# Kernel tuning notes

Measured on AMD Instinct MI355X. Metric: run time of the kernel, lower is better.

## Reference

```python
import jax, jax.numpy as jnp
import numpy as np

B, L, S, H, E, D = 2, 2048, 2048, 16, 64, 64


def setup_inputs() -> dict:
    key = jax.random.key(0)
    kq, kk, kv = jax.random.split(key, 3)
    queries = jax.random.normal(kq, (B, L, H, E), dtype=jnp.float32)
    keys = jax.random.normal(kk, (B, S, H, E), dtype=jnp.float32)
    values = jax.random.normal(kv, (B, S, H, D), dtype=jnp.float32)
    # causal mask: True = masked out (matches masked_fill semantics)
    causal = jnp.triu(jnp.ones((L, S), dtype=bool), k=1)
    attn_mask = jnp.broadcast_to(causal, (B, L, S))
    return {"queries": queries, "keys": keys, "values": values, "attn_mask": attn_mask}


def reference(queries, keys, values, attn_mask):
    # queries: [B,L,H,E], keys: [B,S,H,E], values: [B,S,H,D], attn_mask: [B,L,S] bool
    E_ = queries.shape[-1]
    scale = 1.0 / jnp.sqrt(jnp.asarray(E_, dtype=queries.dtype))
    scores = jnp.einsum('blhe,bshe->bhls', queries, keys)  # [B,H,L,S]
    scores = jnp.where(attn_mask[:, None, :, :], -jnp.inf, scores)
    A = jax.nn.softmax(scale * scores, axis=-1)
    A = jnp.nan_to_num(A)  # fully-masked rows -> 0 (dropout prob is 0.0)
    V = jnp.einsum('bhls,bshd->blhd', A, values)  # [B,L,H,D]
    return (V, A)
```

## Files before the change

kernel.cpp:

```cpp
#include <hip/hip_runtime.h>
#include <cstdint>
#include <cstddef>

#define B_ 2
#define L_ 2048
#define S_ 2048
#define H_ 16
#define E_ 64
#define D_ 64

#define LOG2E_SCALE 0.18033688011112042f

typedef __attribute__((ext_vector_type(8))) short short8;
typedef __attribute__((ext_vector_type(4))) float float4v;
typedef __attribute__((ext_vector_type(4))) unsigned short ushort4v;
typedef __attribute__((ext_vector_type(2))) unsigned int uint2v;

__device__ __forceinline__ unsigned short f2bf(float f) {
  unsigned u = __builtin_bit_cast(unsigned, f);
  u += 0x7FFFu + ((u >> 16) & 1u);
  return (unsigned short)(u >> 16);
}

__device__ __forceinline__ float myexp2(float x) {
#if __has_builtin(__builtin_amdgcn_exp2f)
  return __builtin_amdgcn_exp2f(x);
#else
  return exp2f(x);
#endif
}

__global__ __launch_bounds__(256)
void conv_qk_kernel(const float* __restrict__ Qi, const float* __restrict__ Ki,
                    unsigned short* __restrict__ Qo, unsigned short* __restrict__ Ko) {
  const unsigned bx = blockIdx.x;
  const float* in = (bx & 1u) ? Ki : Qi;
  unsigned short* out = (bx & 1u) ? Ko : Qo;
  unsigned idx4 = (bx >> 1) * 256u + threadIdx.x;
  unsigned e4 = idx4 & 15u;
  unsigned h  = (idx4 >> 4) & 15u;
  unsigned n  = (idx4 >> 8) & 2047u;
  unsigned b  = idx4 >> 19;
  float4v v = *(const float4v*)(in + (size_t)idx4 * 4u);
  ushort4v o;
  o.x = f2bf(v.x); o.y = f2bf(v.y); o.z = f2bf(v.z); o.w = f2bf(v.w);
  *(ushort4v*)(out + (((size_t)(b * H_ + h) * 2048u + n) * 16u + e4) * 4u) = o;
}

__global__ __launch_bounds__(256)
void conv_vt_kernel(const float* __restrict__ V, unsigned short* __restrict__ VT) {
  __shared__ float tile[64 * 65];
  const int st = blockIdx.x, h = blockIdx.y, b = blockIdx.z;
  const int tid = threadIdx.x;
  const float* vb = V + ((size_t)(b * S_ + st * 64) * H_ + h) * D_;
  #pragma unroll
  for (int i = 0; i < 4; ++i) {
    int e = tid + i * 256;
    int row = e >> 4, c4 = (e & 15) * 4;
    float4v v = *(const float4v*)(vb + (size_t)row * (H_ * D_) + c4);
    tile[row * 65 + c4 + 0] = v.x; tile[row * 65 + c4 + 1] = v.y;
    tile[row * 65 + c4 + 2] = v.z; tile[row * 65 + c4 + 3] = v.w;
  }
  __syncthreads();
  #pragma unroll
  for (int i = 0; i < 4; ++i) {
    int e = tid + i * 256;
    int d = e >> 4, c4 = (e & 15) * 4;
    ushort4v o;
    o.x = f2bf(tile[(c4 + 0) * 65 + d]); o.y = f2bf(tile[(c4 + 1) * 65 + d]);
    o.z = f2bf(tile[(c4 + 2) * 65 + d]); o.w = f2bf(tile[(c4 + 3) * 65 + d]);
    *(ushort4v*)(VT + ((size_t)(b * H_ + h) * D_ + d) * S_ + st * 64 + c4) = o;
  }
}

__global__ __launch_bounds__(256, 4)
void fullattn10_kernel(const unsigned short* __restrict__ Qbf,
                       const unsigned short* __restrict__ Kbf,
                       const unsigned short* __restrict__ VT,
                       float* __restrict__ OutV, float* __restrict__ OutA) {
  __shared__ alignas(16) char smem[18944];
  unsigned short* Ps = (unsigned short*)smem;
  float* Lbuf = (float*)(smem + 18432);
  float* Obuf = (float*)smem;

  const int tid = threadIdx.x;
  const int w = tid >> 6;
  const int lane = tid & 63;
  const int quad = lane >> 4;
  const int n16 = lane & 15;

  const unsigned bid = blockIdx.x;
  const unsigned xcd = bid & 7u;
  const unsigned slot = bid >> 3;
  const unsigned g = xcd * 4u + (slot >> 6);
  const unsigned p = slot & 63u;
  const int h = (int)(g & 15u), b = (int)(g >> 4);
  const int stA = (int)p;
  const int stB = 127 - stA;
  const int jtA = stA >> 2, doffA = (stA & 3) * 16;
  const int jtB = stB >> 2, doffB = (stB & 3) * 16;

  const unsigned short* kbase = Kbf + (size_t)(b * H_ + h) * S_ * E_;
  const unsigned short* vbase = VT + (size_t)(b * H_ + h) * D_ * S_;

  float* arowA = OutA + ((size_t)((b * H_ + h) * L_) + stA * 16) * (size_t)S_;
  float* arowB = OutA + ((size_t)((b * H_ + h) * L_) + stB * 16) * (size_t)S_;

  auto zfill = [&](float* arow0, int jt) {
    const int c4start = (jt + 1) * 16;
    #pragma unroll
    for (int i = 0; i < 4; ++i) {
      float4v* rp = (float4v*)(arow0 + (size_t)(w * 4 + i) * S_);
      for (int c4 = c4start + lane; c4 < S_ / 4; c4 += 64) {
        float4v z = {0.f, 0.f, 0.f, 0.f};
        __builtin_nontemporal_store(z, rp + c4);
      }
    }
  };
  zfill(arowA, jtA);
  zfill(arowB, jtB);

  const unsigned short* qrowA = Qbf + ((size_t)(b * H_ + h) * L_ + stA * 16 + n16) * E_;
  const short8 qA0 = *(const short8*)(qrowA + quad * 8);
  const short8 qA1 = *(const short8*)(qrowA + 32 + quad * 8);
  const unsigned short* qrowB = Qbf + ((size_t)(b * H_ + h) * L_ + stB * 16 + n16) * E_;
  const short8 qB0 = *(const short8*)(qrowB + quad * 8);
  const short8 qB1 = *(const short8*)(qrowB + 32 + quad * 8);

  auto pass1 = [&](int jt, int doff, short8 q0, short8 q1) -> float {
    float ls = 0.f;
    short8 kA0[4], kA1[4], kB0[4], kB1[4];
    auto loadK = [&](int j, short8 (&c0)[4], short8 (&c1)[4]) {
      const unsigned short* kb = kbase + (size_t)j * 64 * E_;
      #pragma unroll
      for (int t = 0; t < 4; ++t) {
        const unsigned short* kr = kb + (size_t)(t * 16 + n16) * E_;
        c0[t] = *(const short8*)(kr + quad * 8);
        c1[t] = *(const short8*)(kr + 32 + quad * 8);
      }
    };
    auto procK = [&](const short8 (&c0)[4], const short8 (&c1)[4], int j) {
      #pragma unroll
      for (int t = 0; t < 4; ++t) {
        float4v acc = {0.f, 0.f, 0.f, 0.f};
        acc = __builtin_amdgcn_mfma_f32_16x16x32_bf16(c0[t], q0, acc, 0, 0, 0);
        acc = __builtin_amdgcn_mfma_f32_16x16x32_bf16(c1[t], q1, acc, 0, 0, 0);
        #pragma unroll
        for (int r = 0; r < 4; ++r) {
          float x = acc[r] * LOG2E_SCALE;
          if (j == jt && (t * 16 + quad * 4 + r > doff + n16)) x = -__builtin_inff();
          ls += myexp2(x);
        }
      }
    };
    if (w <= jt) {
      loadK(w, kA0, kA1);
      int j = w;
      for (;;) {
        if (j + 4 <= jt) loadK(j + 4, kB0, kB1);
        procK(kA0, kA1, j);
        j += 4;
        if (j > jt) break;
        if (j + 4 <= jt) loadK(j + 4, kA0, kA1);
        procK(kB0, kB1, j);
        j += 4;
        if (j > jt) break;
      }
    }
    return ls;
  };

  float lsA = pass1(jtA, doffA, qA0, qA1);
  float lsB = pass1(jtB, doffB, qB0, qB1);
  lsA += __shfl_xor(lsA, 16); lsA += __shfl_xor(lsA, 32);
  lsB += __shfl_xor(lsB, 16); lsB += __shfl_xor(lsB, 32);
  if (quad == 0) { Lbuf[w * 16 + n16] = lsA; Lbuf[64 + w * 16 + n16] = lsB; }
  __syncthreads();
  const float invA = 1.0f / (Lbuf[n16] + Lbuf[16 + n16] + Lbuf[32 + n16] + Lbuf[48 + n16]);
  const float invB = 1.0f / (Lbuf[64 + n16] + Lbuf[80 + n16] + Lbuf[96 + n16] + Lbuf[112 + n16]);

  auto pass2 = [&](int jt, int doff, short8 q0, short8 q1, float inv_l,
                   float* arow0, float4v (&oacc)[4]) {
    float* arowL = arow0 + (size_t)n16 * S_ + quad * 4;
    int par = 0;
    for (int j = w; j <= jt; j += 4, par ^= 1) {
      short8 v0f[4], v1f[4];
      #pragma unroll
      for (int t2 = 0; t2 < 4; ++t2) {
        const unsigned short* vr = vbase + (size_t)(t2 * 16 + n16) * S_ + j * 64;
        v0f[t2] = *(const short8*)(vr + quad * 8);
        v1f[t2] = *(const short8*)(vr + 32 + quad * 8);
      }
      const unsigned short* kb = kbase + (size_t)j * 64 * E_;
      unsigned short* psw = Ps + (size_t)((w << 1) | par) * (16 * 72);
      #pragma unroll
      for (int t = 0; t < 4; ++t) {
        const unsigned short* kr = kb + (size_t)(t * 16 + n16) * E_;
        const short8 c0 = *(const short8*)(kr + quad * 8);
        const short8 c1 = *(const short8*)(kr + 32 + quad * 8);
        float4v acc = {0.f, 0.f, 0.f, 0.f};
        acc = __builtin_amdgcn_mfma_f32_16x16x32_bf16(c0, q0, acc, 0, 0, 0);
        acc = __builtin_amdgcn_mfma_f32_16x16x32_bf16(c1, q1, acc, 0, 0, 0);
        float p4v[4];
        #pragma unroll
        for (int r = 0; r < 4; ++r) {
          p4v[r] = myexp2(acc[r] * LOG2E_SCALE) * inv_l;
          if (j == jt && (t * 16 + quad * 4 + r > doff + n16)) p4v[r] = 0.f;
        }
        float4v p4 = {p4v[0], p4v[1], p4v[2], p4v[3]};
        __builtin_nontemporal_store(p4, (float4v*)(arowL + j * 64 + t * 16));
        uint2v dw;
        dw.x = (unsigned)f2bf(p4v[0]) | ((unsigned)f2bf(p4v[1]) << 16);
        dw.y = (unsigned)f2bf(p4v[2]) | ((unsigned)f2bf(p4v[3]) << 16);
        *(uint2v*)&psw[n16 * 72 + t * 16 + quad * 4] = dw;
      }
      __builtin_amdgcn_wave_barrier();
      const short8 aP0 = *(const short8*)&psw[n16 * 72 + quad * 8];
      const short8 aP1 = *(const short8*)&psw[n16 * 72 + 32 + quad * 8];
      #pragma unroll
      for (int t2 = 0; t2 < 4; ++t2) {
        oacc[t2] = __builtin_amdgcn_mfma_f32_16x16x32_bf16(aP0, v0f[t2], oacc[t2], 0, 0, 0);
        oacc[t2] = __builtin_amdgcn_mfma_f32_16x16x32_bf16(aP1, v1f[t2], oacc[t2], 0, 0, 0);
      }
    }
  };

  auto combineO = [&](int l0, float4v (&oacc)[4]) {
    __syncthreads();
    #pragma unroll
    for (int t2 = 0; t2 < 4; ++t2)
      #pragma unroll
      for (int r = 0; r < 4; ++r)
        Obuf[(size_t)(w * 16 + quad * 4 + r) * 68 + t2 * 16 + n16] = oacc[t2][r];
    __syncthreads();
    const int row = tid >> 4;
    const int c0 = (tid & 15) * 4;
    float4v s = *(const float4v*)&Obuf[(size_t)row * 68 + c0];
    #pragma unroll
    for (int ww = 1; ww < 4; ++ww) {
      float4v t = *(const float4v*)&Obuf[(size_t)(ww * 16 + row) * 68 + c0];
      s.x += t.x; s.y += t.y; s.z += t.z; s.w += t.w;
    }
    float* op = OutV + ((size_t)(b * L_ + l0 + row) * H_ + h) * D_ + c0;
    __builtin_nontemporal_store(s, (float4v*)op);
    __syncthreads();
  };

  float4v oacc[4];
  #pragma unroll
  for (int t2 = 0; t2 < 4; ++t2) oacc[t2] = (float4v){0.f, 0.f, 0.f, 0.f};
  pass2(jtA, doffA, qA0, qA1, invA, arowA, oacc);
  combineO(stA * 16, oacc);

  #pragma unroll
  for (int t2 = 0; t2 < 4; ++t2) oacc[t2] = (float4v){0.f, 0.f, 0.f, 0.f};
  pass2(jtB, doffB, qB0, qB1, invB, arowB, oacc);
  combineO(stB * 16, oacc);
}

__global__ __launch_bounds__(256, 4)
void fullattn_fb_kernel(const float* __restrict__ Q, const float* __restrict__ K,
                        const float* __restrict__ V, float* __restrict__ OutV,
                        float* __restrict__ OutA) {
  __shared__ alignas(16) unsigned short Qs[64 * 72];
  __shared__ alignas(16) unsigned short Ks[64 * 72];
  __shared__ alignas(16) unsigned short VTs[64 * 72];
  __shared__ alignas(16) unsigned short Ps[64 * 72];
  const int tid = threadIdx.x;
  const int w = tid >> 6, lane = tid & 63, quad = lane >> 4, n16 = lane & 15;
  const int lt = (int)(gridDim.x - 1u - blockIdx.x);
  const int h = blockIdx.y, b = blockIdx.z;
  const int l0 = lt * 64;
  float* arow0 = OutA + ((size_t)((b * H_ + h) * L_) + l0) * (size_t)S_;
  {
    const int c4start = (lt + 1) * 16;
    for (int rr = w; rr < 64; rr += 4) {
      float4v* rp = (float4v*)(arow0 + (size_t)rr * S_);
      for (int c4 = c4start + lane; c4 < S_ / 4; c4 += 64) {
        float4v z = {0.f, 0.f, 0.f, 0.f};
        __builtin_nontemporal_store(z, rp + c4);
      }
    }
  }
  {
    const float* qb = Q + ((size_t)(b * L_ + l0) * H_ + h) * E_;
    #pragma unroll
    for (int i = 0; i < 4; ++i) {
      int e = tid + i * 256;
      int row = e >> 4, c4 = (e & 15) * 4;
      float4v qv = *(const float4v*)(qb + (size_t)row * (H_ * E_) + c4);
      ushort4v o; o.x = f2bf(qv.x); o.y = f2bf(qv.y); o.z = f2bf(qv.z); o.w = f2bf(qv.w);
      *(ushort4v*)&Qs[row * 72 + c4] = o;
    }
  }
  auto stageK = [&](int j) {
    const float* kb = K + ((size_t)(b * S_ + j * 64) * H_ + h) * E_;
    #pragma unroll
    for (int i = 0; i < 4; ++i) {
      int e = tid + i * 256;
      int row = e >> 4, c4 = (e & 15) * 4;
      float4v kv = *(const float4v*)(kb + (size_t)row * (H_ * E_) + c4);
      ushort4v o; o.x = f2bf(kv.x); o.y = f2bf(kv.y); o.z = f2bf(kv.z); o.w = f2bf(kv.w);
      *(ushort4v*)&Ks[row * 72 + c4] = o;
    }
  };
  auto stageV = [&](int j) {
    const float* vb = V + ((size_t)(b * S_ + j * 64) * H_ + h) * D_;
    const int d = lane;
    #pragma unroll
    for (int i = 0; i < 8; ++i) {
      int s2 = w * 8 + i;
      float f0 = vb[(size_t)(2 * s2) * (H_ * D_) + d];
      float f1 = vb[(size_t)(2 * s2 + 1) * (H_ * D_) + d];
      unsigned pk = (unsigned)f2bf(f0) | ((unsigned)f2bf(f1) << 16);
      *(unsigned*)&VTs[d * 72 + 2 * s2] = pk;
    }
  };
  __syncthreads();
  const short8 aQ0 = *(const short8*)&Qs[(w * 16 + n16) * 72 + quad * 8];
  const short8 aQ1 = *(const short8*)&Qs[(w * 16 + n16) * 72 + 32 + quad * 8];
  float m2[4], lsum[4];
  #pragma unroll
  for (int r = 0; r < 4; ++r) { m2[r] = -__builtin_inff(); lsum[r] = 0.f; }
  for (int j = 0; j <= lt; ++j) {
    stageK(j);
    __syncthreads();
    float x[4][4];
    #pragma unroll
    for (int t = 0; t < 4; ++t) {
      const short8 b0 = *(const short8*)&Ks[(t * 16 + n16) * 72 + quad * 8];
      const short8 b1 = *(const short8*)&Ks[(t * 16 + n16) * 72 + 32 + quad * 8];
      float4v acc = {0.f, 0.f, 0.f, 0.f};
      acc = __builtin_amdgcn_mfma_f32_16x16x32_bf16(aQ0, b0, acc, 0, 0, 0);
      acc = __builtin_amdgcn_mfma_f32_16x16x32_bf16(aQ1, b1, acc, 0, 0, 0);
      #pragma unroll
      for (int r = 0; r < 4; ++r) x[t][r] = acc[r] * LOG2E_SCALE;
    }
    if (j == lt) {
      #pragma unroll
      for (int t = 0; t < 4; ++t)
        #pragma unroll
        for (int r = 0; r < 4; ++r)
          if (t * 16 + n16 > w * 16 + quad * 4 + r) x[t][r] = -__builtin_inff();
    }
    #pragma unroll
    for (int r = 0; r < 4; ++r) {
      float mx = fmaxf(fmaxf(x[0][r], x[1][r]), fmaxf(x[2][r], x[3][r]));
      #pragma unroll
      for (int off = 8; off >= 1; off >>= 1) mx = fmaxf(mx, __shfl_xor(mx, off));
      float mnew = fmaxf(m2[r], mx);
      float alpha = myexp2(m2[r] - mnew);
      float sm = myexp2(x[0][r] - mnew) + myexp2(x[1][r] - mnew) +
                 myexp2(x[2][r] - mnew) + myexp2(x[3][r] - mnew);
      #pragma unroll
      for (int off = 8; off >= 1; off >>= 1) sm += __shfl_xor(sm, off);
      lsum[r] = lsum[r] * alpha + sm;
      m2[r] = mnew;
    }
    __syncthreads();
  }
  float inv_l[4];
  #pragma unroll
  for (int r = 0; r < 4; ++r) inv_l[r] = 1.0f / lsum[r];
  float4v oacc[4];
  #pragma unroll
  for (int t2 = 0; t2 < 4; ++t2) oacc[t2] = (float4v){0.f, 0.f, 0.f, 0.f};
  for (int j = 0; j <= lt; ++j) {
    stageK(j);
    stageV(j);
    __syncthreads();
    float* arow = arow0 + (size_t)(w * 16 + quad * 4) * S_ + j * 64 + n16;
    #pragma unroll
    for (int t = 0; t < 4; ++t) {
      const short8 b0 = *(const short8*)&Ks[(t * 16 + n16) * 72 + quad * 8];
      const short8 b1 = *(const short8*)&Ks[(t * 16 + n16) * 72 + 32 + quad * 8];
      float4v acc = {0.f, 0.f, 0.f, 0.f};
      acc = __builtin_amdgcn_mfma_f32_16x16x32_bf16(aQ0, b0, acc, 0, 0, 0);
      acc = __builtin_amdgcn_mfma_f32_16x16x32_bf16(aQ1, b1, acc, 0, 0, 0);
      #pragma unroll
      for (int r = 0; r < 4; ++r) {
        float p = myexp2(acc[r] * LOG2E_SCALE - m2[r]) * inv_l[r];
        if (j == lt && (t * 16 + n16 > w * 16 + quad * 4 + r)) p = 0.f;
        __builtin_nontemporal_store(p, arow + (size_t)r * S_ + t * 16);
        float pp = __shfl_xor(p, 1);
        unsigned short sp = f2bf(p), spp = f2bf(pp);
        unsigned dw = (n16 & 1) ? ((unsigned)spp | ((unsigned)sp << 16))
                                : ((unsigned)sp | ((unsigned)spp << 16));
        *(unsigned*)&Ps[(w * 16 + quad * 4 + r) * 72 + (t * 16 + (n16 & ~1))] = dw;
      }
    }
    __builtin_amdgcn_wave_barrier();
    const short8 aP0 = *(const short8*)&Ps[(w * 16 + n16) * 72 + quad * 8];
    const short8 aP1 = *(const short8*)&Ps[(w * 16 + n16) * 72 + 32 + quad * 8];
    #pragma unroll
    for (int t2 = 0; t2 < 4; ++t2) {
      const short8 v0 = *(const short8*)&VTs[(t2 * 16 + n16) * 72 + quad * 8];
      const short8 v1 = *(const short8*)&VTs[(t2 * 16 + n16) * 72 + 32 + quad * 8];
      oacc[t2] = __builtin_amdgcn_mfma_f32_16x16x32_bf16(aP0, v0, oacc[t2], 0, 0, 0);
      oacc[t2] = __builtin_amdgcn_mfma_f32_16x16x32_bf16(aP1, v1, oacc[t2], 0, 0, 0);
    }
    __syncthreads();
  }
  float* ob = OutV + ((size_t)(b * L_ + l0 + w * 16 + quad * 4) * H_ + h) * D_ + n16;
  #pragma unroll
  for (int t2 = 0; t2 < 4; ++t2)
    #pragma unroll
    for (int r = 0; r < 4; ++r)
      __builtin_nontemporal_store(oacc[t2][r], ob + (size_t)r * (H_ * D_) + t2 * 16);
}

extern "C" void kernel_launch(void* const* d_in, const int* in_sizes, int n_in,
                              void* d_out, int out_size, void* d_ws, size_t ws_size,
                              hipStream_t stream) {
  (void)in_sizes; (void)n_in; (void)out_size;
  const float* Q = (const float*)d_in[0];
  const float* K = (const float*)d_in[1];
  const float* V = (const float*)d_in[2];
  float* OutV = (float*)d_out;
  float* OutA = (float*)d_out + (size_t)B_ * L_ * H_ * D_;

  const size_t bytes_each = (size_t)B_ * H_ * 2048 * 64 * sizeof(unsigned short);
  if (ws_size >= 3 * bytes_each) {
    unsigned short* Qbf = (unsigned short*)d_ws;
    unsigned short* Kbf = (unsigned short*)((char*)d_ws + bytes_each);
    unsigned short* VTb = (unsigned short*)((char*)d_ws + 2 * bytes_each);
    const int nblk = (B_ * 2048 * H_ * E_ / 4) / 256;
    conv_qk_kernel<<<2 * nblk, 256, 0, stream>>>(Q, K, Qbf, Kbf);
    conv_vt_kernel<<<dim3(S_ / 64, H_, B_), 256, 0, stream>>>(V, VTb);
    fullattn10_kernel<<<2048, 256, 0, stream>>>(Qbf, Kbf, VTb, OutV, OutA);
  } else {
    fullattn_fb_kernel<<<dim3(L_ / 64, H_, B_), 256, 0, stream>>>(Q, K, V, OutV, OutA);
  }
}
```

Baseline: 739.4 us.

## Split softmax-denominator pass into separate kernel with workspace row sums

The fused attention kernel is split in two. A lightweight lpass_kernel computes the softmax denominators, writes their reciprocals to a workspace buffer and does the zero-fill of the masked upper triangle. The main kernel then reads those reciprocals and does only the probability/PV pass. The aim is to raise occupancy and shrink register pressure per kernel, with launch bounds of 8 and 5 instead of 4. It also drops the manual K double-buffering and the XCD-aware block remapping in favour of a plain 3D grid. The cost is an extra launch, a small workspace round trip, and a larger workspace requirement that could route to the fallback path if the workspace is too small.

After: 733.3 us. Within noise of the previous version (-0.8%).

```diff
diff --git a/kernel.cpp b/kernel.cpp
--- a/kernel.cpp
+++ b/kernel.cpp
@@ -73,15 +73,11 @@
   }
 }
 
-__global__ __launch_bounds__(256, 4)
-void fullattn10_kernel(const unsigned short* __restrict__ Qbf,
-                       const unsigned short* __restrict__ Kbf,
-                       const unsigned short* __restrict__ VT,
-                       float* __restrict__ OutV, float* __restrict__ OutA) {
-  __shared__ alignas(16) char smem[18944];
-  unsigned short* Ps = (unsigned short*)smem;
-  float* Lbuf = (float*)(smem + 18432);
-  float* Obuf = (float*)smem;
+__global__ __launch_bounds__(256, 8)
+void lpass_kernel(const unsigned short* __restrict__ Qbf,
+                  const unsigned short* __restrict__ Kbf,
+                  float* __restrict__ Lws, float* __restrict__ OutA) {
+  __shared__ float Lbuf[128];
 
   const int tid = threadIdx.x;
   const int w = tid >> 6;
@@ -89,20 +85,13 @@
   const int quad = lane >> 4;
   const int n16 = lane & 15;
 
-  const unsigned bid = blockIdx.x;
-  const unsigned xcd = bid & 7u;
-  const unsigned slot = bid >> 3;
-  const unsigned g = xcd * 4u + (slot >> 6);
-  const unsigned p = slot & 63u;
-  const int h = (int)(g & 15u), b = (int)(g >> 4);
-  const int stA = (int)p;
+  const int h = blockIdx.y, b = blockIdx.z;
+  const int stA = (int)blockIdx.x;
   const int stB = 127 - stA;
   const int jtA = stA >> 2, doffA = (stA & 3) * 16;
   const int jtB = stB >> 2, doffB = (stB & 3) * 16;
 
   const unsigned short* kbase = Kbf + (size_t)(b * H_ + h) * S_ * E_;
-  const unsigned short* vbase = VT + (size_t)(b * H_ + h) * D_ * S_;
-
   float* arowA = OutA + ((size_t)((b * H_ + h) * L_) + stA * 16) * (size_t)S_;
   float* arowB = OutA + ((size_t)((b * H_ + h) * L_) + stB * 16) * (size_t)S_;
 
@@ -120,31 +109,20 @@
   zfill(arowA, jtA);
   zfill(arowB, jtB);
 
-  const unsigned short* qrowA = Qbf + ((size_t)(b * H_ + h) * L_ + stA * 16 + n16) * E_;
-  const short8 qA0 = *(const short8*)(qrowA + quad * 8);
-  const short8 qA1 = *(const short8*)(qrowA + 32 + quad * 8);
-  const unsigned short* qrowB = Qbf + ((size_t)(b * H_ + h) * L_ + stB * 16 + n16) * E_;
-  const short8 qB0 = *(const short8*)(qrowB + quad * 8);
-  const short8 qB1 = *(const short8*)(qrowB + 32 + quad * 8);
-
-  auto pass1 = [&](int jt, int doff, short8 q0, short8 q1) -> float {
+  auto pass1 = [&](int jt, int doff, const unsigned short* qrow) -> float {
+    const short8 q0 = *(const short8*)(qrow + quad * 8);
+    const short8 q1 = *(const short8*)(qrow + 32 + quad * 8);
     float ls = 0.f;
-    short8 kA0[4], kA1[4], kB0[4], kB1[4];
-    auto loadK = [&](int j, short8 (&c0)[4], short8 (&c1)[4]) {
+    for (int j = w; j <= jt; j += 4) {
       const unsigned short* kb = kbase + (size_t)j * 64 * E_;
       #pragma unroll
       for (int t = 0; t < 4; ++t) {
         const unsigned short* kr = kb + (size_t)(t * 16 + n16) * E_;
-        c0[t] = *(const short8*)(kr + quad * 8);
-        c1[t] = *(const short8*)(kr + 32 + quad * 8);
-      }
-    };
-    auto procK = [&](const short8 (&c0)[4], const short8 (&c1)[4], int j) {
-      #pragma unroll
-      for (int t = 0; t < 4; ++t) {
+        const short8 c0 = *(const short8*)(kr + quad * 8);
+        const short8 c1 = *(const short8*)(kr + 32 + quad * 8);
         float4v acc = {0.f, 0.f, 0.f, 0.f};
-        acc = __builtin_amdgcn_mfma_f32_16x16x32_bf16(c0[t], q0, acc, 0, 0, 0);
-        acc = __builtin_amdgcn_mfma_f32_16x16x32_bf16(c1[t], q1, acc, 0, 0, 0);
+        acc = __builtin_amdgcn_mfma_f32_16x16x32_bf16(c0, q0, acc, 0, 0, 0);
+        acc = __builtin_amdgcn_mfma_f32_16x16x32_bf16(c1, q1, acc, 0, 0, 0);
         #pragma unroll
         for (int r = 0; r < 4; ++r) {
           float x = acc[r] * LOG2E_SCALE;
@@ -152,35 +130,61 @@
           ls += myexp2(x);
         }
       }
-    };
-    if (w <= jt) {
-      loadK(w, kA0, kA1);
-      int j = w;
-      for (;;) {
-        if (j + 4 <= jt) loadK(j + 4, kB0, kB1);
-        procK(kA0, kA1, j);
-        j += 4;
-        if (j > jt) break;
-        if (j + 4 <= jt) loadK(j + 4, kA0, kA1);
-        procK(kB0, kB1, j);
-        j += 4;
-        if (j > jt) break;
-      }
     }
     return ls;
   };
 
-  float lsA = pass1(jtA, doffA, qA0, qA1);
-  float lsB = pass1(jtB, doffB, qB0, qB1);
+  const unsigned short* qbase = Qbf + (size_t)(b * H_ + h) * L_ * E_;
+  float lsA = pass1(jtA, doffA, qbase + (size_t)(stA * 16 + n16) * E_);
+  float lsB = pass1(jtB, doffB, qbase + (size_t)(stB * 16 + n16) * E_);
   lsA += __shfl_xor(lsA, 16); lsA += __shfl_xor(lsA, 32);
   lsB += __shfl_xor(lsB, 16); lsB += __shfl_xor(lsB, 32);
   if (quad == 0) { Lbuf[w * 16 + n16] = lsA; Lbuf[64 + w * 16 + n16] = lsB; }
   __syncthreads();
-  const float invA = 1.0f / (Lbuf[n16] + Lbuf[16 + n16] + Lbuf[32 + n16] + Lbuf[48 + n16]);
-  const float invB = 1.0f / (Lbuf[64 + n16] + Lbuf[80 + n16] + Lbuf[96 + n16] + Lbuf[112 + n16]);
-
-  auto pass2 = [&](int jt, int doff, short8 q0, short8 q1, float inv_l,
-                   float* arow0, float4v (&oacc)[4]) {
+  if (tid < 32) {
+    const int row = tid & 15, s = tid >> 4;
+    const float* lb = Lbuf + s * 64;
+    const float sum = lb[row] + lb[16 + row] + lb[32 + row] + lb[48 + row];
+    const int st = s ? stB : stA;
+    Lws[(size_t)(b * H_ + h) * L_ + st * 16 + row] = 1.0f / sum;
+  }
+}
+
+__global__ __launch_bounds__(256, 5)
+void fullattn11_kernel(const unsigned short* __restrict__ Qbf,
+                       const unsigned short* __restrict__ Kbf,
+                       const unsigned short* __restrict__ VT,
+                       const float* __restrict__ Lws,
+                       float* __restrict__ OutV, float* __restrict__ OutA) {
+  __shared__ alignas(16) char smem[18432];
+  unsigned short* Ps = (unsigned short*)smem;
+  float* Obuf = (float*)smem;
+
+  const int tid = threadIdx.x;
+  const int w = tid >> 6;
+  const int lane = tid & 63;
+  const int quad = lane >> 4;
+  const int n16 = lane & 15;
+
+  const int h = blockIdx.y, b = blockIdx.z;
+  const int stA = (int)blockIdx.x;
+  const int stB = 127 - stA;
+  const int jtA = stA >> 2, doffA = (stA & 3) * 16;
+  const int jtB = stB >> 2, doffB = (stB & 3) * 16;
+
+  const unsigned short* kbase = Kbf + (size_t)(b * H_ + h) * S_ * E_;
+  const unsigned short* vbase = VT + (size_t)(b * H_ + h) * D_ * S_;
+  const unsigned short* qbase = Qbf + (size_t)(b * H_ + h) * L_ * E_;
+  const float* lrow = Lws + (size_t)(b * H_ + h) * L_;
+
+  float* arowA = OutA + ((size_t)((b * H_ + h) * L_) + stA * 16) * (size_t)S_;
+  float* arowB = OutA + ((size_t)((b * H_ + h) * L_) + stB * 16) * (size_t)S_;
+
+  auto pass2 = [&](int jt, int doff, int st, float* arow0, float4v (&oacc)[4]) {
+    const unsigned short* qrow = qbase + (size_t)(st * 16 + n16) * E_;
+    const short8 q0 = *(const short8*)(qrow + quad * 8);
+    const short8 q1 = *(const short8*)(qrow + 32 + quad * 8);
+    const float inv_l = lrow[st * 16 + n16];
     float* arowL = arow0 + (size_t)n16 * S_ + quad * 4;
     int par = 0;
     for (int j = w; j <= jt; j += 4, par ^= 1) {
@@ -249,12 +253,12 @@
   float4v oacc[4];
   #pragma unroll
   for (int t2 = 0; t2 < 4; ++t2) oacc[t2] = (float4v){0.f, 0.f, 0.f, 0.f};
-  pass2(jtA, doffA, qA0, qA1, invA, arowA, oacc);
+  pass2(jtA, doffA, stA, arowA, oacc);
   combineO(stA * 16, oacc);
 
   #pragma unroll
   for (int t2 = 0; t2 < 4; ++t2) oacc[t2] = (float4v){0.f, 0.f, 0.f, 0.f};
-  pass2(jtB, doffB, qB0, qB1, invB, arowB, oacc);
+  pass2(jtB, doffB, stB, arowB, oacc);
   combineO(stB * 16, oacc);
 }
 
@@ -420,14 +424,17 @@
   float* OutA = (float*)d_out + (size_t)B_ * L_ * H_ * D_;
 
   const size_t bytes_each = (size_t)B_ * H_ * 2048 * 64 * sizeof(unsigned short);
-  if (ws_size >= 3 * bytes_each) {
+  const size_t lbytes = (size_t)B_ * H_ * L_ * sizeof(float);
+  if (ws_size >= 3 * bytes_each + lbytes) {
     unsigned short* Qbf = (unsigned short*)d_ws;
     unsigned short* Kbf = (unsigned short*)((char*)d_ws + bytes_each);
     unsigned short* VTb = (unsigned short*)((char*)d_ws + 2 * bytes_each);
+    float* Lws = (float*)((char*)d_ws + 3 * bytes_each);
     const int nblk = (B_ * 2048 * H_ * E_ / 4) / 256;
     conv_qk_kernel<<<2 * nblk, 256, 0, stream>>>(Q, K, Qbf, Kbf);
+    lpass_kernel<<<dim3(64, H_, B_), 256, 0, stream>>>(Qbf, Kbf, Lws, OutA);
     conv_vt_kernel<<<dim3(S_ / 64, H_, B_), 256, 0, stream>>>(V, VTb);
-    fullattn10_kernel<<<2048, 256, 0, stream>>>(Qbf, Kbf, VTb, OutV, OutA);
+    fullattn11_kernel<<<dim3(64, H_, B_), 256, 0, stream>>>(Qbf, Kbf, VTb, Lws, OutV, OutA);
   } else {
     fullattn_fb_kernel<<<dim3(L_ / 64, H_, B_), 256, 0, stream>>>(Q, K, V, OutV, OutA);
   }
```
